# Kernel optimization log

Hardware: AMD Instinct MI355X
Metric: run time of the kernel (lower is better)

The kernel has to match this reference:

```python
import jax, jax.numpy as jnp
import numpy as np

N, D, H, DH = 8192, 512, 8, 64          # seq len, model dim, heads, head dim
NF = int(DH * math_log) if False else 266  # nb_features = int(64 * ln(64)) = 266
EPS = 1e-4                               # performer softmax-kernel eps
LN_EPS = 1e-5


def layernorm(x, g, b):
    mu = x.mean(-1, keepdims=True)
    var = ((x - mu) ** 2).mean(-1, keepdims=True)
    return (x - mu) * jax.lax.rsqrt(var + LN_EPS) * g + b


def softmax_kernel(data, proj, is_query):
    # data: [b,h,n,dh], proj: [nf,dh] -> phi(data): [b,h,n,nf]
    dnorm = DH ** -0.25
    ratio = NF ** -0.5
    dd = jnp.einsum('bhnd,jd->bhnj', data * dnorm, proj)
    diag = (data ** 2).sum(-1, keepdims=True) * 0.5 * (dnorm ** 2)
    if is_query:
        m = jnp.max(dd, axis=-1, keepdims=True)
    else:
        m = jnp.max(dd, axis=(-1, -2), keepdims=True)
    return ratio * (jnp.exp(dd - diag - m) + EPS)


def setup_inputs() -> dict:
    key = jax.random.key(0)
    ks = jax.random.split(key, 10)
    s = 0.02
    return {
        'x': jax.random.normal(ks[0], (N, D), jnp.float32),
        'proj': jax.random.normal(ks[1], (NF, DH), jnp.float32),
        'ln1_g': jnp.ones((D,), jnp.float32), 'ln1_b': jnp.zeros((D,), jnp.float32),
        'wq': jax.random.normal(ks[2], (D, D), jnp.float32) * s,
        'wk': jax.random.normal(ks[3], (D, D), jnp.float32) * s,
        'wv': jax.random.normal(ks[4], (D, D), jnp.float32) * s,
        'wo': jax.random.normal(ks[5], (D, D), jnp.float32) * s,
        'wo_b': jnp.zeros((D,), jnp.float32),
        'ln2_g': jnp.ones((D,), jnp.float32), 'ln2_b': jnp.zeros((D,), jnp.float32),
        'w1': jax.random.normal(ks[6], (D, 4 * D), jnp.float32) * s,
        'b1': jnp.zeros((4 * D,), jnp.float32),
        'w2': jax.random.normal(ks[7], (4 * D, D), jnp.float32) * s,
        'b2': jnp.zeros((D,), jnp.float32),
    }


def reference(x, proj, ln1_g, ln1_b, wq, wk, wv, wo, wo_b, ln2_g, ln2_b, w1, b1, w2, b2):
    xb = x[None]                                     # [1,N,D] (the unsqueeze(0))
    # --- PreLN FAVOR+ self-attention ---
    h = layernorm(xb, ln1_g, ln1_b)
    def split_heads(t):
        return t.reshape(1, N, H, DH).transpose(0, 2, 1, 3)   # [1,H,N,DH]
    q = split_heads(h @ wq)
    k = split_heads(h @ wk)
    v = split_heads(h @ wv)
    qp = softmax_kernel(q, proj, True)               # [1,H,N,NF]
    kp = softmax_kernel(k, proj, False)              # [1,H,N,NF]
    # non-causal linear attention
    context = jnp.einsum('bhnj,bhnd->bhjd', kp, v)   # [1,H,NF,DH]
    d_inv = 1.0 / jnp.einsum('bhnj,bhj->bhn', qp, kp.sum(axis=2))
    attn = jnp.einsum('bhnj,bhjd->bhnd', qp, context) * d_inv[..., None]
    attn = attn.transpose(0, 2, 1, 3).reshape(1, N, D)
    xb = xb + attn @ wo + wo_b
    # --- PreLN feed-forward (GELU, mult=4) ---
    h2 = layernorm(xb, ln2_g, ln2_b)
    xb = xb + jax.nn.gelu(h2 @ w1 + b1) @ w2 + b2
    return xb[0]                                     # squeeze -> [N,D]
```

## Files before the change

### kernel.cpp

```cpp
#include <hip/hip_runtime.h>
#include <math.h>


typedef __attribute__((ext_vector_type(8))) short bf16x8;
typedef __attribute__((ext_vector_type(4))) float f32x4;

#define N_SEQ 8192
#define DMODEL 512
#define DQKV 1536
#define NHEAD 8
#define DHEAD 64
#define NF 266
#define NFP 320
#define PEPS 1e-4f
#define LNEPS 1e-5f
#define RATIO 0.06131393694f

__device__ __forceinline__ unsigned short f2bf(float f) {
  unsigned u = __float_as_uint(f);
  u += 0x7FFFu + ((u >> 16) & 1u);
  return (unsigned short)(u >> 16);
}
__device__ __forceinline__ float bf2f(unsigned short b) {
  return __uint_as_float(((unsigned)b) << 16);
}
__device__ __forceinline__ unsigned enc_f32(float f) {
  unsigned i = __float_as_uint(f);
  return (i & 0x80000000u) ? ~i : (i | 0x80000000u);
}
__device__ __forceinline__ float dec_f32(unsigned u) {
  return (u & 0x80000000u) ? __uint_as_float(u & 0x7FFFFFFFu) : __uint_as_float(~u);
}

__device__ __forceinline__ void g2l16(const void* g, void* l) {
  __builtin_amdgcn_global_load_lds(
      (const __attribute__((address_space(1))) void*)g,
      (__attribute__((address_space(3))) void*)l, 16, 0, 0);
}

template <int N>
__device__ __forceinline__ void wait_vmcnt() {
  if constexpr (N == 0) asm volatile("s_waitcnt vmcnt(0)" ::: "memory");
  else if constexpr (N == 5) asm volatile("s_waitcnt vmcnt(5)" ::: "memory");
  else if constexpr (N == 6) asm volatile("s_waitcnt vmcnt(6)" ::: "memory");
}
__device__ __forceinline__ void wait_lgkm0() {
  asm volatile("s_waitcnt lgkmcnt(0)" ::: "memory");
}


__global__ __launch_bounds__(256) void prep_kernel(
    const float* __restrict__ wq, const float* __restrict__ wk,
    const float* __restrict__ wv, const float* __restrict__ wo,
    const float* __restrict__ w1, const float* __restrict__ w2,
    const float* __restrict__ proj,
    unsigned short* __restrict__ wtqkv, unsigned short* __restrict__ wot,
    unsigned short* __restrict__ w1t, unsigned short* __restrict__ w2t,
    unsigned short* __restrict__ pb, unsigned* __restrict__ mk,
    const float* __restrict__ x,
    const float* __restrict__ ln1g, const float* __restrict__ ln1b,
    unsigned short* __restrict__ h_bf) {
  int bid = blockIdx.x;
  if (bid < 3072) {
    const float* src; unsigned short* dst; int R, C, base;
    if (bid < 256)       { src = wq; dst = wtqkv;          R = 512;  C = 512;  base = 0; }
    else if (bid < 512)  { src = wk; dst = wtqkv + 262144; R = 512;  C = 512;  base = 256; }
    else if (bid < 768)  { src = wv; dst = wtqkv + 524288; R = 512;  C = 512;  base = 512; }
    else if (bid < 1024) { src = wo; dst = wot;            R = 512;  C = 512;  base = 768; }
    else if (bid < 2048) { src = w1; dst = w1t;            R = 512;  C = 2048; base = 1024; }
    else                 { src = w2; dst = w2t;            R = 2048; C = 512;  base = 2048; }
    int lb = bid - base;
    int nbx = C / 32;
    int c0 = (lb % nbx) * 32, r0 = (lb / nbx) * 32;
    __shared__ float tile[32][33];
    int tx = threadIdx.x & 31, ty = threadIdx.x >> 5;
    #pragma unroll
    for (int i = ty; i < 32; i += 8)
      tile[i][tx] = src[(long)(r0 + i) * C + c0 + tx];
    __syncthreads();
    #pragma unroll
    for (int i = ty; i < 32; i += 8)
      dst[(long)(c0 + i) * R + r0 + tx] = f2bf(tile[tx][i]);
  } else if (bid < 3152) {
    int id = (bid - 3072) * 256 + threadIdx.x;
    int j = id >> 6;
    pb[id] = (j < NF) ? f2bf(proj[(long)j * 64 + (id & 63)] * 0.35355339059327373f)
                      : (unsigned short)0;
  } else if (bid == 3152) {
    if (threadIdx.x < NHEAD) mk[threadIdx.x] = 0x007FFFFFu;
  } else {
    __shared__ float sred[4];
    int row = bid - 3153, t = threadIdx.x;
    float2 v = ((const float2*)(x + (long)row * DMODEL))[t];
    float s = v.x + v.y;
    #pragma unroll
    for (int m = 32; m >= 1; m >>= 1) s += __shfl_xor(s, m);
    if ((t & 63) == 0) sred[t >> 6] = s;
    __syncthreads();
    float mu = (sred[0] + sred[1] + sred[2] + sred[3]) * (1.0f / DMODEL);
    __syncthreads();
    float d0 = v.x - mu, d1 = v.y - mu;
    float q = d0 * d0 + d1 * d1;
    #pragma unroll
    for (int m = 32; m >= 1; m >>= 1) q += __shfl_xor(q, m);
    if ((t & 63) == 0) sred[t >> 6] = q;
    __syncthreads();
    float var = (sred[0] + sred[1] + sred[2] + sred[3]) * (1.0f / DMODEL);
    float inv = rsqrtf(var + LNEPS);
    int c = t * 2;
    unsigned short o0 = f2bf(d0 * inv * ln1g[c] + ln1b[c]);
    unsigned short o1 = f2bf(d1 * inv * ln1g[c + 1] + ln1b[c + 1]);
    ((unsigned*)(h_bf + (long)row * DMODEL))[t] = ((unsigned)o1 << 16) | o0;
  }
}


__global__ __launch_bounds__(256) void ln_kernel(const float* __restrict__ x,
                                                 const float* __restrict__ g,
                                                 const float* __restrict__ b,
                                                 unsigned short* __restrict__ out) {
  __shared__ float sred[4];
  int row = blockIdx.x, t = threadIdx.x;
  float2 v = ((const float2*)(x + (long)row * DMODEL))[t];
  float s = v.x + v.y;
  #pragma unroll
  for (int m = 32; m >= 1; m >>= 1) s += __shfl_xor(s, m);
  if ((t & 63) == 0) sred[t >> 6] = s;
  __syncthreads();
  float mu = (sred[0] + sred[1] + sred[2] + sred[3]) * (1.0f / DMODEL);
  __syncthreads();
  float d0 = v.x - mu, d1 = v.y - mu;
  float q = d0 * d0 + d1 * d1;
  #pragma unroll
  for (int m = 32; m >= 1; m >>= 1) q += __shfl_xor(q, m);
  if ((t & 63) == 0) sred[t >> 6] = q;
  __syncthreads();
  float var = (sred[0] + sred[1] + sred[2] + sred[3]) * (1.0f / DMODEL);
  float inv = rsqrtf(var + LNEPS);
  int c = t * 2;
  unsigned short o0 = f2bf(d0 * inv * g[c] + b[c]);
  unsigned short o1 = f2bf(d1 * inv * g[c + 1] + b[c + 1]);
  ((unsigned*)(out + (long)row * DMODEL))[t] = ((unsigned)o1 << 16) | o0;
}

enum { EPI_BF16 = 0, EPI_BIAS_RES_F32 = 2, EPI_BIAS_GELU = 3, EPI_QKV = 4 };


template <int EPI>
__global__ __launch_bounds__(512, 4) void gemm8w_kernel(
    const unsigned short* __restrict__ A, int lda,
    const unsigned short* __restrict__ Bt, int ldb,
    void* __restrict__ Cv, int ldc,
    int K,
    const float* __restrict__ bias,
    const float* __restrict__ res, int ldr,
    unsigned short* __restrict__ vt) {
  constexpr int MR = 4, NR = 2;
  constexpr int S = 5;
  const int tid = threadIdx.x;
  const int wave = tid >> 6, lane = tid & 63;
  const int lr = lane & 15, lg = lane >> 4;
  const int wr = wave >> 1, wc = wave & 1;
  const int m0 = blockIdx.x * 256, n0 = blockIdx.y * 64;

  __shared__ uint4 a_s[2][2048];
  __shared__ uint4 b_s[2][512];

  const unsigned short* asrc[4];
  #pragma unroll
  for (int e = 0; e < 4; ++e) {
    int chunk = e * 512 + tid;
    int r = chunk >> 3, c = chunk & 7;
    asrc[e] = A + (long)(m0 + r) * lda + (c ^ (r & 7)) * 8;
  }
  const unsigned short* bsrc;
  {
    int r = tid >> 3, c = tid & 7;
    bsrc = Bt + (long)(n0 + r) * ldb + (c ^ (r & 7)) * 8;
  }
  const int wbase = tid & 448;

  f32x4 acc[MR][NR] = {};

  auto stage = [&](int buf, int t) {
    #pragma unroll
    for (int e = 0; e < 4; ++e)
      g2l16(asrc[e] + t * 64, &a_s[buf][e * 512 + wbase]);
    g2l16(bsrc + t * 64, &b_s[buf][wbase]);
  };
  auto compute = [&](int buf) {
    #pragma unroll
    for (int ks = 0; ks < 2; ++ks) {
      bf16x8 af[MR], bv[NR];
      #pragma unroll
      for (int i = 0; i < MR; ++i) {
        int r = wr * 64 + i * 16 + lr;
        af[i] = *(const bf16x8*)&a_s[buf][r * 8 + ((ks * 4 + lg) ^ (r & 7))];
      }
      #pragma unroll
      for (int j = 0; j < NR; ++j) {
        int r = wc * 32 + j * 16 + lr;
        bv[j] = *(const bf16x8*)&b_s[buf][r * 8 + ((ks * 4 + lg) ^ (r & 7))];
      }
      #pragma unroll
      for (int i = 0; i < MR; ++i)
        #pragma unroll
        for (int j = 0; j < NR; ++j)
          acc[i][j] = __builtin_amdgcn_mfma_f32_16x16x32_bf16(af[i], bv[j], acc[i][j], 0, 0, 0);
    }
  };

  const int NT = K >> 6;
  stage(0, 0);
  stage(1, 1);
  wait_vmcnt<S>();
  __builtin_amdgcn_s_barrier();

  int cur = 0;
  for (int t = 0; t < NT; ++t) {
    compute(cur);
    if (t + 1 < NT) {
      wait_lgkm0();
      __builtin_amdgcn_s_barrier();
      if (t + 2 < NT) {
        stage(cur, t + 2);
        wait_vmcnt<S>();
      } else {
        wait_vmcnt<0>();
      }
      __builtin_amdgcn_s_barrier();
    }
    cur ^= 1;
  }

  #pragma unroll
  for (int i = 0; i < MR; ++i) {
    #pragma unroll
    for (int j = 0; j < NR; ++j) {
      int gn = n0 + wc * 32 + j * 16 + lr;
      int gm0 = m0 + wr * 64 + i * 16 + lg * 4;
      if (EPI == EPI_QKV && gn >= 1024) {
        int d = gn - 1024;
        uint2 u;
        u.x = (unsigned)f2bf(acc[i][j][0]) | ((unsigned)f2bf(acc[i][j][1]) << 16);
        u.y = (unsigned)f2bf(acc[i][j][2]) | ((unsigned)f2bf(acc[i][j][3]) << 16);
        *(uint2*)(vt + (long)d * N_SEQ + gm0) = u;
        continue;
      }
      #pragma unroll
      for (int rg = 0; rg < 4; ++rg) {
        int gm = gm0 + rg;
        float v = acc[i][j][rg];
        if (EPI == EPI_BF16 || EPI == EPI_QKV) {
          ((unsigned short*)Cv)[(long)gm * ldc + gn] = f2bf(v);
        } else if (EPI == EPI_BIAS_RES_F32) {
          v += bias[gn] + res[(long)gm * ldr + gn];
          ((float*)Cv)[(long)gm * ldc + gn] = v;
        } else if (EPI == EPI_BIAS_GELU) {
          v += bias[gn];
          float t3 = 0.7978845608028654f * (v + 0.044715f * v * v * v);
          v = v / (1.0f + __expf(-2.0f * t3));
          ((unsigned short*)Cv)[(long)gm * ldc + gn] = f2bf(v);
        }
      }
    }
  }
}


template <int BM, int BN, int WM, int WN, int EPI>
__global__ __launch_bounds__(256) void gemm_kernel(
    const unsigned short* __restrict__ A, int lda,
    const unsigned short* __restrict__ Bt, int ldb,
    void* __restrict__ Cv, int ldc,
    int K,
    const float* __restrict__ bias,
    const float* __restrict__ res, int ldr) {
  static_assert((BM / WM) * (BN / WN) == 4, "need 4 waves");
  constexpr int MR = WM / 16, NR = WN / 16;
  constexpr int WNN = BN / WN;
  constexpr int AIT = BM * 8 / 256;
  constexpr int BIT = BN * 8 / 256;
  constexpr int S = AIT + BIT;
  static_assert(S == 6, "wait count tuned for BM=128,BN=64");
  const int tid = threadIdx.x;
  const int wave = tid >> 6, lane = tid & 63;
  const int lr = lane & 15, lg = lane >> 4;
  const int wr = wave / WNN, wc = wave % WNN;
  const int m0 = blockIdx.x * BM, n0 = blockIdx.y * BN;

  __shared__ uint4 a_s[2][BM * 8];
  __shared__ uint4 b_s[2][BN * 8];

  const unsigned short* asrc[AIT];
  #pragma unroll
  for (int e = 0; e < AIT; ++e) {
    int chunk = e * 256 + tid;
    int r = chunk >> 3, c = chunk & 7;
    asrc[e] = A + (long)(m0 + r) * lda + (c ^ (r & 7)) * 8;
  }
  const unsigned short* bsrc[BIT];
  #pragma unroll
  for (int e = 0; e < BIT; ++e) {
    int chunk = e * 256 + tid;
    int r = chunk >> 3, c = chunk & 7;
    bsrc[e] = Bt + (long)(n0 + r) * ldb + (c ^ (r & 7)) * 8;
  }
  const int wbase = tid & 192;

  f32x4 acc[MR][NR] = {};

  auto stage = [&](int buf, int t) {
    #pragma unroll
    for (int e = 0; e < AIT; ++e)
      g2l16(asrc[e] + t * 64, &a_s[buf][e * 256 + wbase]);
    #pragma unroll
    for (int e = 0; e < BIT; ++e)
      g2l16(bsrc[e] + t * 64, &b_s[buf][e * 256 + wbase]);
  };
  auto compute = [&](int buf) {
    #pragma unroll
    for (int ks = 0; ks < 2; ++ks) {
      bf16x8 af[MR], bv[NR];
      #pragma unroll
      for (int i = 0; i < MR; ++i) {
        int r = wr * WM + i * 16 + lr;
        af[i] = *(const bf16x8*)&a_s[buf][r * 8 + ((ks * 4 + lg) ^ (r & 7))];
      }
      #pragma unroll
      for (int j = 0; j < NR; ++j) {
        int r = wc * WN + j * 16 + lr;
        bv[j] = *(const bf16x8*)&b_s[buf][r * 8 + ((ks * 4 + lg) ^ (r & 7))];
      }
      #pragma unroll
      for (int i = 0; i < MR; ++i)
        #pragma unroll
        for (int j = 0; j < NR; ++j)
          acc[i][j] = __builtin_amdgcn_mfma_f32_16x16x32_bf16(af[i], bv[j], acc[i][j], 0, 0, 0);
    }
  };

  const int NT = K >> 6;
  stage(0, 0);
  stage(1, 1);
  wait_vmcnt<6>();
  __builtin_amdgcn_s_barrier();

  int cur = 0;
  for (int t = 0; t < NT; ++t) {
    compute(cur);
    if (t + 1 < NT) {
      wait_lgkm0();
      __builtin_amdgcn_s_barrier();
      if (t + 2 < NT) {
        stage(cur, t + 2);
        wait_vmcnt<6>();
      } else {
        wait_vmcnt<0>();
      }
      __builtin_amdgcn_s_barrier();
    }
    cur ^= 1;
  }

  #pragma unroll
  for (int i = 0; i < MR; ++i) {
    #pragma unroll
    for (int j = 0; j < NR; ++j) {
      int gn = n0 + wc * WN + j * 16 + lr;
      #pragma unroll
      for (int rg = 0; rg < 4; ++rg) {
        int gm = m0 + wr * WM + i * 16 + lg * 4 + rg;
        float v = acc[i][j][rg];
        if (EPI == EPI_BF16) {
          ((unsigned short*)Cv)[(long)gm * ldc + gn] = f2bf(v);
        } else if (EPI == EPI_BIAS_RES_F32) {
          v += bias[gn] + res[(long)gm * ldr + gn];
          ((float*)Cv)[(long)gm * ldc + gn] = v;
        } else if (EPI == EPI_BIAS_GELU) {
          v += bias[gn];
          float t3 = 0.7978845608028654f * (v + 0.044715f * v * v * v);
          v = v / (1.0f + __expf(-2.0f * t3));
          ((unsigned short*)Cv)[(long)gm * ldc + gn] = f2bf(v);
        }
      }
    }
  }
}


__global__ __launch_bounds__(256) void kmax_kernel(
    const unsigned short* __restrict__ Kp,
    const unsigned short* __restrict__ pb,
    unsigned* __restrict__ mk) {
  const int tid = threadIdx.x;
  const int wave = tid >> 6, lane = tid & 63;
  const int lr = lane & 15, lg = lane >> 4;
  const int h = blockIdx.z;
  const int m0 = blockIdx.x * 256;
  const int wbase = tid & 192;

  __shared__ uint4 pbs[2560];
  __shared__ uint4 abuf[2][512];
  __shared__ float sred[4];

  #pragma unroll
  for (int e = 0; e < 10; ++e) {
    int chunk = e * 256 + tid;
    int r = chunk >> 3, c = chunk & 7;
    g2l16(pb + (long)r * DHEAD + (c ^ (r & 7)) * 8, pbs + e * 256 + wbase);
  }
  auto stage_a = [&](int b, int sub) {
    #pragma unroll
    for (int e = 0; e < 2; ++e) {
      int chunk = e * 256 + tid;
      int r = chunk >> 3, c = chunk & 7;
      g2l16(Kp + (long)(m0 + sub * 64 + r) * DQKV + h * DHEAD + (c ^ (r & 7)) * 8,
            abuf[b] + e * 256 + wbase);
    }
  };

  stage_a(0, 0);
  __syncthreads();

  float m = -3.0e38f;
  for (int sub = 0; sub < 4; ++sub) {
    const int cur = sub & 1;
    if (sub + 1 < 4) stage_a(cur ^ 1, sub + 1);

    f32x4 acc[17] = {};
    #pragma unroll
    for (int ks = 0; ks < 2; ++ks) {
      int rA = wave * 16 + lr;
      bf16x8 af = *(const bf16x8*)&abuf[cur][rA * 8 + ((ks * 4 + lg) ^ (rA & 7))];
      #pragma unroll
      for (int j = 0; j < 17; ++j) {
        int rB = j * 16 + lr;
        bf16x8 bv = *(const bf16x8*)&pbs[rB * 8 + ((ks * 4 + lg) ^ (rB & 7))];
        acc[j] = __builtin_amdgcn_mfma_f32_16x16x32_bf16(af, bv, acc[j], 0, 0, 0);
      }
    }
    #pragma unroll
    for (int j = 0; j < 17; ++j) {
      bool valid = (j < 16) || (lr < 10);
      if (valid) {
        #pragma unroll
        for (int rg = 0; rg < 4; ++rg) m = fmaxf(m, acc[j][rg]);
      }
    }
    if (sub + 1 < 4) __syncthreads();
  }

  #pragma unroll
  for (int s = 1; s < 64; s <<= 1) m = fmaxf(m, __shfl_xor(m, s));
  if (lane == 0) sred[wave] = m;
  __syncthreads();
  if (tid == 0) {
    float mm = fmaxf(fmaxf(sred[0], sred[1]), fmaxf(sred[2], sred[3]));
    atomicMax(&mk[h], enc_f32(mm));
  }
}


__global__ __launch_bounds__(256) void ctx_fused_kernel(
    const unsigned short* __restrict__ Kp,
    const unsigned short* __restrict__ pb,
    const unsigned short* __restrict__ vT,
    const unsigned* __restrict__ mk,
    float* __restrict__ part,
    float* __restrict__ kspart) {
  const int tid = threadIdx.x;
  const int wave = tid >> 6, lane = tid & 63;
  const int lr = lane & 15, lg = lane >> 4;
  const int kc = blockIdx.x, h = blockIdx.y;
  const int wbase = tid & 192;

  __shared__ uint4 smem[7168];
  uint4* pbs = smem;
  auto kbuf = [&](int b) { return smem + 2560 + b * 512; };
  auto vbuf = [&](int b) { return smem + 3584 + b * 512; };
  uint4* Pt = smem + 4608;

  #pragma unroll
  for (int e = 0; e < 10; ++e) {
    int chunk = e * 256 + tid;
    int r = chunk >> 3, c = chunk & 7;
    g2l16(pb + (long)r * DHEAD + (c ^ (r & 7)) * 8, pbs + e * 256 + wbase);
  }

  auto stage_kv = [&](int b, int sub) {
    int n0 = kc * 256 + sub * 64;
    #pragma unroll
    for (int e = 0; e < 2; ++e) {
      int chunk = e * 256 + tid;
      int r = chunk >> 3, c = chunk & 7;
      g2l16(Kp + (long)(n0 + r) * DQKV + h * DHEAD + (c ^ (r & 7)) * 8,
            kbuf(b) + e * 256 + wbase);
      g2l16(vT + ((long)h * DHEAD + r) * N_SEQ + n0 + (c ^ (r & 7)) * 8,
            vbuf(b) + e * 256 + wbase);
    }
  };

  const float mh = dec_f32(mk[h]);
  f32x4 acc2[2][10] = {};
  float colacc[20];
  #pragma unroll
  for (int j = 0; j < 20; ++j) colacc[j] = 0.f;

  const int wr = wave >> 1, wc = wave & 1;

  stage_kv(0, 0);
  for (int sub = 0; sub < 4; ++sub) {
    const int cur = sub & 1;
    __syncthreads();
    if (sub + 1 < 4) stage_kv(cur ^ 1, sub + 1);

    f32x4 acc[20] = {};
    float qs = 0.f;
    #pragma unroll
    for (int ks = 0; ks < 2; ++ks) {
      int rA = wave * 16 + lr;
      bf16x8 af = *(const bf16x8*)&kbuf(cur)[rA * 8 + ((ks * 4 + lg) ^ (rA & 7))];
      #pragma unroll
      for (int i = 0; i < 8; ++i) {
        float f = bf2f((unsigned short)af[i]);
        qs += f * f;
      }
      #pragma unroll
      for (int j = 0; j < 20; ++j) {
        int rB = j * 16 + lr;
        bf16x8 bv = *(const bf16x8*)&pbs[rB * 8 + ((ks * 4 + lg) ^ (rB & 7))];
        acc[j] = __builtin_amdgcn_mfma_f32_16x16x32_bf16(af, bv, acc[j], 0, 0, 0);
      }
    }
    qs += __shfl_xor(qs, 16);
    qs += __shfl_xor(qs, 32);
    float dg[4];
    #pragma unroll
    for (int rg = 0; rg < 4; ++rg) dg[rg] = 0.0625f * __shfl(qs, lg * 4 + rg);

    __syncthreads();

    unsigned short* Ptu = (unsigned short*)Pt;
    const int nrow = wave * 16 + lg * 4;
    #pragma unroll
    for (int j = 0; j < 20; ++j) {
      int colj = j * 16 + lr;
      #pragma unroll
      for (int rg = 0; rg < 4; ++rg) {
        float v = 0.f;
        if (colj < NF) v = RATIO * (__expf(acc[j][rg] - dg[rg] - mh) + PEPS);
        colacc[j] += v;
        int nr = nrow + rg;
        int idx = ((colj * 8 + ((nr >> 3) ^ (colj & 7))) << 3) + (nr & 7);
        Ptu[idx] = f2bf(v);
      }
    }
    __syncthreads();

    #pragma unroll
    for (int ks = 0; ks < 2; ++ks) {
      bf16x8 af[2], bv[10];
      #pragma unroll
      for (int i = 0; i < 2; ++i) {
        int r = wr * 32 + i * 16 + lr;
        af[i] = *(const bf16x8*)&vbuf(cur)[r * 8 + ((ks * 4 + lg) ^ (r & 7))];
      }
      #pragma unroll
      for (int j = 0; j < 10; ++j) {
        int r = wc * 160 + j * 16 + lr;
        bv[j] = *(const bf16x8*)&Pt[r * 8 + ((ks * 4 + lg) ^ (r & 7))];
      }
      #pragma unroll
      for (int i = 0; i < 2; ++i)
        #pragma unroll
        for (int j = 0; j < 10; ++j)
          acc2[i][j] = __builtin_amdgcn_mfma_f32_16x16x32_bf16(af[i], bv[j], acc2[i][j], 0, 0, 0);
    }
  }

  float* pbase = part + ((long)(h * 32 + kc)) * 64 * NFP;
  #pragma unroll
  for (int i = 0; i < 2; ++i) {
    #pragma unroll
    for (int j = 0; j < 10; ++j) {
      int gn = wc * 160 + j * 16 + lr;
      #pragma unroll
      for (int rg = 0; rg < 4; ++rg) {
        int gm = wr * 32 + i * 16 + lg * 4 + rg;
        pbase[(long)gm * NFP + gn] = acc2[i][j][rg];
      }
    }
  }

  __syncthreads();
  float* kls = (float*)Pt;
  #pragma unroll
  for (int j = 0; j < 20; ++j) {
    float cs = colacc[j];
    cs += __shfl_xor(cs, 16);
    cs += __shfl_xor(cs, 32);
    if (lg == 0) kls[wave * NFP + j * 16 + lr] = cs;
  }
  __syncthreads();
  for (int c0 = tid; c0 < NFP; c0 += 256) {
    kspart[((long)(h * 32 + kc)) * NFP + c0] =
        kls[c0] + kls[NFP + c0] + kls[2 * NFP + c0] + kls[3 * NFP + c0];
  }
}


__global__ void ctx_reduce_kernel(const float* __restrict__ part,
                                  const float* __restrict__ kspart,
                                  unsigned short* __restrict__ ctxpad) {
  int i = blockIdx.x * 256 + threadIdx.x;
  int h = i / (96 * NFP);
  int rem = i % (96 * NFP);
  int r = rem / NFP, j = rem % NFP;
  float s = 0.f;
  if (r < 64) {
    #pragma unroll 4
    for (int kc = 0; kc < 32; ++kc)
      s += part[((long)(h * 32 + kc)) * 64 * NFP + r * NFP + j];
  } else if (r == 64) {
    #pragma unroll 4
    for (int kc = 0; kc < 32; ++kc)
      s += kspart[((long)(h * 32 + kc)) * NFP + j];
  }
  ctxpad[i] = f2bf(s);
}


__global__ __launch_bounds__(256) void attn_fused_kernel(
    const unsigned short* __restrict__ Qp,
    const unsigned short* __restrict__ pb,
    const unsigned short* __restrict__ ctxpad,
    unsigned short* __restrict__ attn) {
  const int tid = threadIdx.x;
  const int wave = tid >> 6, lane = tid & 63;
  const int lr = lane & 15, lg = lane >> 4;
  const int h = blockIdx.z;
  const int m0 = blockIdx.x * 64;
  const int wbase = tid & 192;

  __shared__ uint4 smem[4096];
  auto sbuf = [&](int b) { return smem + b * 768; };
  uint4* Pf = smem + 1536;

  const unsigned short* Aq = Qp + (long)m0 * DQKV + h * DHEAD;
  const unsigned short* Ch = ctxpad + (long)h * 96 * NFP;

  auto stage_ctx = [&](int b, int kk) {
    #pragma unroll
    for (int e = 0; e < 3; ++e) {
      int chunk = e * 256 + tid;
      int r = chunk >> 3, c = chunk & 7;
      g2l16(Ch + (long)r * NFP + kk * 64 + (c ^ (r & 7)) * 8, sbuf(b) + e * 256 + wbase);
    }
  };

  #pragma unroll
  for (int e = 0; e < 2; ++e) {
    int chunk = e * 256 + tid;
    int r = chunk >> 3, c = chunk & 7;
    g2l16(Aq + (long)r * DQKV + (c ^ (r & 7)) * 8, sbuf(0) + e * 256 + wbase);
  }
  #pragma unroll
  for (int e = 0; e < 10; ++e) {
    int chunk = e * 256 + tid;
    int r = chunk >> 3, c = chunk & 7;
    g2l16(pb + (long)r * DHEAD + (c ^ (r & 7)) * 8, Pf + e * 256 + wbase);
  }
  __syncthreads();

  f32x4 acc[20] = {};
  float qs = 0.f;
  #pragma unroll
  for (int ks = 0; ks < 2; ++ks) {
    int rA = wave * 16 + lr;
    bf16x8 af = *(const bf16x8*)&sbuf(0)[rA * 8 + ((ks * 4 + lg) ^ (rA & 7))];
    #pragma unroll
    for (int i = 0; i < 8; ++i) {
      float f = bf2f((unsigned short)af[i]);
      qs += f * f;
    }
    #pragma unroll
    for (int j = 0; j < 20; ++j) {
      int rB = j * 16 + lr;
      bf16x8 bv = *(const bf16x8*)&Pf[rB * 8 + ((ks * 4 + lg) ^ (rB & 7))];
      acc[j] = __builtin_amdgcn_mfma_f32_16x16x32_bf16(af, bv, acc[j], 0, 0, 0);
    }
  }
  qs += __shfl_xor(qs, 16);
  qs += __shfl_xor(qs, 32);
  float dg[4];
  #pragma unroll
  for (int rg = 0; rg < 4; ++rg) dg[rg] = 0.0625f * __shfl(qs, lg * 4 + rg);

  float mrow[4];
  #pragma unroll
  for (int rg = 0; rg < 4; ++rg) mrow[rg] = -3.0e38f;
  #pragma unroll
  for (int j = 0; j < 17; ++j) {
    bool valid = (j < 16) || (lr < 10);
    if (valid) {
      #pragma unroll
      for (int rg = 0; rg < 4; ++rg) mrow[rg] = fmaxf(mrow[rg], acc[j][rg]);
    }
  }
  #pragma unroll
  for (int s = 1; s < 16; s <<= 1)
    #pragma unroll
    for (int rg = 0; rg < 4; ++rg) mrow[rg] = fmaxf(mrow[rg], __shfl_xor(mrow[rg], s));

  __syncthreads();
  stage_ctx(0, 0);

  unsigned short* Pu = (unsigned short*)Pf;
  const int prow = wave * 16 + lg * 4;
  #pragma unroll
  for (int j = 0; j < 20; ++j) {
    int col = j * 16 + lr;
    int kk = col >> 6, cc = (col >> 3) & 7;
    #pragma unroll
    for (int rg = 0; rg < 4; ++rg) {
      float v = 0.f;
      if (col < NF) v = RATIO * (__expf(acc[j][rg] - dg[rg] - mrow[rg]) + PEPS);
      int rw = prow + rg;
      int idx = ((kk * 512 + rw * 8 + (cc ^ (rw & 7))) << 3) + (col & 7);
      Pu[idx] = f2bf(v);
    }
  }
  __syncthreads();

  f32x4 acc2[6] = {};
  #pragma unroll
  for (int kk = 0; kk < 5; ++kk) {
    const int cur = kk & 1;
    if (kk + 1 < 5) stage_ctx(cur ^ 1, kk + 1);
    #pragma unroll
    for (int ks = 0; ks < 2; ++ks) {
      int rA = wave * 16 + lr;
      bf16x8 af = *(const bf16x8*)&Pf[kk * 512 + rA * 8 + ((ks * 4 + lg) ^ (rA & 7))];
      #pragma unroll
      for (int j = 0; j < 6; ++j) {
        int rB = j * 16 + lr;
        bf16x8 bv = *(const bf16x8*)&sbuf(cur)[rB * 8 + ((ks * 4 + lg) ^ (rB & 7))];
        acc2[j] = __builtin_amdgcn_mfma_f32_16x16x32_bf16(af, bv, acc2[j], 0, 0, 0);
      }
    }
    if (kk + 1 < 5) __syncthreads();
  }

  #pragma unroll
  for (int rg = 0; rg < 4; ++rg) {
    float dv = __shfl(acc2[4][rg], lane & 48);
    float inv = 1.0f / dv;
    int gm = m0 + wave * 16 + lg * 4 + rg;
    #pragma unroll
    for (int j = 0; j < 4; ++j) {
      attn[(long)gm * DMODEL + h * DHEAD + j * 16 + lr] = f2bf(acc2[j][rg] * inv);
    }
  }
}


extern "C" void kernel_launch(void* const* d_in, const int* in_sizes, int n_in,
                              void* d_out, int out_size, void* d_ws, size_t ws_size,
                              hipStream_t stream) {
  const float* x    = (const float*)d_in[0];
  const float* proj = (const float*)d_in[1];
  const float* ln1g = (const float*)d_in[2];
  const float* ln1b = (const float*)d_in[3];
  const float* wq   = (const float*)d_in[4];
  const float* wk   = (const float*)d_in[5];
  const float* wv   = (const float*)d_in[6];
  const float* wo   = (const float*)d_in[7];
  const float* wob  = (const float*)d_in[8];
  const float* ln2g = (const float*)d_in[9];
  const float* ln2b = (const float*)d_in[10];
  const float* w1   = (const float*)d_in[11];
  const float* b1   = (const float*)d_in[12];
  const float* w2   = (const float*)d_in[13];
  const float* b2   = (const float*)d_in[14];

  char* ws = (char*)d_ws;
  unsigned short* wtqkv = (unsigned short*)(ws + 0);
  unsigned short* wot   = (unsigned short*)(ws + 1572864);
  unsigned short* w1t   = (unsigned short*)(ws + 2097152);
  unsigned short* w2t   = (unsigned short*)(ws + 4194304);
  unsigned short* pb    = (unsigned short*)(ws + 6291456);
  unsigned short* h_bf  = (unsigned short*)(ws + 6332416);
  unsigned short* qkv   = (unsigned short*)(ws + 14721024);
  unsigned* mk          = (unsigned*)(ws + 124297216);
  unsigned short* vT    = (unsigned short*)(ws + 124297472);
  float* part           = (float*)(ws + 132686080);
  float* kspart         = (float*)(ws + 153657600);
  unsigned short* ctxpad= (unsigned short*)(ws + 154978560);
  unsigned short* gbf   = (unsigned short*)(ws + 130468096);
  unsigned short* attn  = h_bf;
  unsigned short* h2    = qkv;
  float* xb             = (float*)d_out;

  dim3 blk(256);

  prep_kernel<<<11345, blk, 0, stream>>>(wq, wk, wv, wo, w1, w2, proj,
                                         wtqkv, wot, w1t, w2t, pb, mk,
                                         x, ln1g, ln1b, h_bf);

  gemm8w_kernel<EPI_QKV><<<dim3(32, 24), dim3(512), 0, stream>>>(
      h_bf, 512, wtqkv, 512, qkv, DQKV, 512, nullptr, nullptr, 0, vT);

  kmax_kernel<<<dim3(32, 1, 8), blk, 0, stream>>>(qkv + 512, pb, mk);

  ctx_fused_kernel<<<dim3(32, 8), blk, 0, stream>>>(qkv + 512, pb, vT, mk, part, kspart);
  ctx_reduce_kernel<<<960, blk, 0, stream>>>(part, kspart, ctxpad);

  attn_fused_kernel<<<dim3(128, 1, 8), blk, 0, stream>>>(qkv, pb, ctxpad, attn);

  gemm_kernel<128, 64, 64, 32, EPI_BIAS_RES_F32><<<dim3(64, 8), blk, 0, stream>>>(
      attn, 512, wot, 512, xb, 512, 512, wob, x, 512);

  ln_kernel<<<N_SEQ, blk, 0, stream>>>(xb, ln2g, ln2b, h2);

  gemm8w_kernel<EPI_BIAS_GELU><<<dim3(32, 32), dim3(512), 0, stream>>>(
      h2, 512, w1t, 512, gbf, 2048, 512, b1, nullptr, 0, nullptr);

  gemm8w_kernel<EPI_BIAS_RES_F32><<<dim3(32, 8), dim3(512), 0, stream>>>(
      gbf, 2048, w2t, 2048, d_out, 512, 2048, b2, xb, 512, nullptr);
}
```

Measured before the change: 179.8 us.

## Use wave-per-row layernorm, shrink ctx LDS, switch FFN2 to smaller-tile GEMM

LayerNorm now processes one row per wavefront with float4 loads and shuffle-only reductions, dropping shared-memory syncs and cutting the block count by four. The context kernel drops K/V double buffering and splits the P tile into two halves, shrinking LDS so two blocks can fit per CU, at the cost of losing load/compute overlap. The final FFN down-projection moves from the 8-wave GEMM to the 128x64 tile GEMM, launching more blocks to fill the device better.

After: 168.4 us. 1.07x faster.

```diff
diff --git a/kernel.cpp b/kernel.cpp
--- a/kernel.cpp
+++ b/kernel.cpp
@@ -46,6 +46,38 @@
 }
 __device__ __forceinline__ void wait_lgkm0() {
   asm volatile("s_waitcnt lgkmcnt(0)" ::: "memory");
+}
+
+
+__device__ __forceinline__ void ln_row(const float* __restrict__ x,
+                                       const float* __restrict__ g,
+                                       const float* __restrict__ b,
+                                       unsigned short* __restrict__ out,
+                                       long row, int lane) {
+  const float4* xr = (const float4*)(x + row * DMODEL);
+  float4 v0 = xr[lane * 2], v1 = xr[lane * 2 + 1];
+  float s = v0.x + v0.y + v0.z + v0.w + v1.x + v1.y + v1.z + v1.w;
+  #pragma unroll
+  for (int m = 32; m >= 1; m >>= 1) s += __shfl_xor(s, m);
+  float mu = s * (1.0f / DMODEL);
+  float d[8] = {v0.x - mu, v0.y - mu, v0.z - mu, v0.w - mu,
+                v1.x - mu, v1.y - mu, v1.z - mu, v1.w - mu};
+  float q = 0.f;
+  #pragma unroll
+  for (int k = 0; k < 8; ++k) q += d[k] * d[k];
+  #pragma unroll
+  for (int m = 32; m >= 1; m >>= 1) q += __shfl_xor(q, m);
+  float inv = rsqrtf(q * (1.0f / DMODEL) + LNEPS);
+  const float4* gr = (const float4*)g;
+  const float4* br = (const float4*)b;
+  float4 g0 = gr[lane * 2], g1 = gr[lane * 2 + 1];
+  float4 b0 = br[lane * 2], b1 = br[lane * 2 + 1];
+  float gg[8] = {g0.x, g0.y, g0.z, g0.w, g1.x, g1.y, g1.z, g1.w};
+  float bb[8] = {b0.x, b0.y, b0.z, b0.w, b1.x, b1.y, b1.z, b1.w};
+  unsigned short o[8];
+  #pragma unroll
+  for (int k = 0; k < 8; ++k) o[k] = f2bf(d[k] * inv * gg[k] + bb[k]);
+  ((uint4*)(out + row * DMODEL))[lane] = *(uint4*)o;
 }
 
 
@@ -89,28 +121,8 @@
   } else if (bid == 3152) {
     if (threadIdx.x < NHEAD) mk[threadIdx.x] = 0x007FFFFFu;
   } else {
-    __shared__ float sred[4];
-    int row = bid - 3153, t = threadIdx.x;
-    float2 v = ((const float2*)(x + (long)row * DMODEL))[t];
-    float s = v.x + v.y;
-    #pragma unroll
-    for (int m = 32; m >= 1; m >>= 1) s += __shfl_xor(s, m);
-    if ((t & 63) == 0) sred[t >> 6] = s;
-    __syncthreads();
-    float mu = (sred[0] + sred[1] + sred[2] + sred[3]) * (1.0f / DMODEL);
-    __syncthreads();
-    float d0 = v.x - mu, d1 = v.y - mu;
-    float q = d0 * d0 + d1 * d1;
-    #pragma unroll
-    for (int m = 32; m >= 1; m >>= 1) q += __shfl_xor(q, m);
-    if ((t & 63) == 0) sred[t >> 6] = q;
-    __syncthreads();
-    float var = (sred[0] + sred[1] + sred[2] + sred[3]) * (1.0f / DMODEL);
-    float inv = rsqrtf(var + LNEPS);
-    int c = t * 2;
-    unsigned short o0 = f2bf(d0 * inv * ln1g[c] + ln1b[c]);
-    unsigned short o1 = f2bf(d1 * inv * ln1g[c + 1] + ln1b[c + 1]);
-    ((unsigned*)(h_bf + (long)row * DMODEL))[t] = ((unsigned)o1 << 16) | o0;
+    long row = (long)(bid - 3153) * 4 + (threadIdx.x >> 6);
+    ln_row(x, ln1g, ln1b, h_bf, row, threadIdx.x & 63);
   }
 }
 
@@ -119,28 +131,8 @@
                                                  const float* __restrict__ g,
                                                  const float* __restrict__ b,
                                                  unsigned short* __restrict__ out) {
-  __shared__ float sred[4];
-  int row = blockIdx.x, t = threadIdx.x;
-  float2 v = ((const float2*)(x + (long)row * DMODEL))[t];
-  float s = v.x + v.y;
-  #pragma unroll
-  for (int m = 32; m >= 1; m >>= 1) s += __shfl_xor(s, m);
-  if ((t & 63) == 0) sred[t >> 6] = s;
-  __syncthreads();
-  float mu = (sred[0] + sred[1] + sred[2] + sred[3]) * (1.0f / DMODEL);
-  __syncthreads();
-  float d0 = v.x - mu, d1 = v.y - mu;
-  float q = d0 * d0 + d1 * d1;
-  #pragma unroll
-  for (int m = 32; m >= 1; m >>= 1) q += __shfl_xor(q, m);
-  if ((t & 63) == 0) sred[t >> 6] = q;
-  __syncthreads();
-  float var = (sred[0] + sred[1] + sred[2] + sred[3]) * (1.0f / DMODEL);
-  float inv = rsqrtf(var + LNEPS);
-  int c = t * 2;
-  unsigned short o0 = f2bf(d0 * inv * g[c] + b[c]);
-  unsigned short o1 = f2bf(d1 * inv * g[c + 1] + b[c + 1]);
-  ((unsigned*)(out + (long)row * DMODEL))[t] = ((unsigned)o1 << 16) | o0;
+  long row = (long)blockIdx.x * 4 + (threadIdx.x >> 6);
+  ln_row(x, g, b, out, row, threadIdx.x & 63);
 }
 
 enum { EPI_BF16 = 0, EPI_BIAS_RES_F32 = 2, EPI_BIAS_GELU = 3, EPI_QKV = 4 };
@@ -462,7 +454,7 @@
 }
 
 
-__global__ __launch_bounds__(256) void ctx_fused_kernel(
+__global__ __launch_bounds__(256, 2) void ctx_fused_kernel(
     const unsigned short* __restrict__ Kp,
     const unsigned short* __restrict__ pb,
     const unsigned short* __restrict__ vT,
@@ -475,11 +467,11 @@
   const int kc = blockIdx.x, h = blockIdx.y;
   const int wbase = tid & 192;
 
-  __shared__ uint4 smem[7168];
-  uint4* pbs = smem;
-  auto kbuf = [&](int b) { return smem + 2560 + b * 512; };
-  auto vbuf = [&](int b) { return smem + 3584 + b * 512; };
-  uint4* Pt = smem + 4608;
+  __shared__ uint4 smem[4864];
+  uint4* pbs  = smem;
+  uint4* kstg = smem + 2560;
+  uint4* vstg = smem + 3072;
+  uint4* Pt   = smem + 3584;
 
   #pragma unroll
   for (int e = 0; e < 10; ++e) {
@@ -488,39 +480,34 @@
     g2l16(pb + (long)r * DHEAD + (c ^ (r & 7)) * 8, pbs + e * 256 + wbase);
   }
 
-  auto stage_kv = [&](int b, int sub) {
-    int n0 = kc * 256 + sub * 64;
+  const float mh = dec_f32(mk[h]);
+  f32x4 acc2[2][10] = {};
+  float colacc[20];
+  #pragma unroll
+  for (int j = 0; j < 20; ++j) colacc[j] = 0.f;
+
+  const int wr = wave >> 1, wc = wave & 1;
+
+  for (int sub = 0; sub < 4; ++sub) {
+    const int n0 = kc * 256 + sub * 64;
+    __syncthreads();
     #pragma unroll
     for (int e = 0; e < 2; ++e) {
       int chunk = e * 256 + tid;
       int r = chunk >> 3, c = chunk & 7;
       g2l16(Kp + (long)(n0 + r) * DQKV + h * DHEAD + (c ^ (r & 7)) * 8,
-            kbuf(b) + e * 256 + wbase);
+            kstg + e * 256 + wbase);
       g2l16(vT + ((long)h * DHEAD + r) * N_SEQ + n0 + (c ^ (r & 7)) * 8,
-            vbuf(b) + e * 256 + wbase);
-    }
-  };
-
-  const float mh = dec_f32(mk[h]);
-  f32x4 acc2[2][10] = {};
-  float colacc[20];
-  #pragma unroll
-  for (int j = 0; j < 20; ++j) colacc[j] = 0.f;
-
-  const int wr = wave >> 1, wc = wave & 1;
-
-  stage_kv(0, 0);
-  for (int sub = 0; sub < 4; ++sub) {
-    const int cur = sub & 1;
+            vstg + e * 256 + wbase);
+    }
     __syncthreads();
-    if (sub + 1 < 4) stage_kv(cur ^ 1, sub + 1);
 
     f32x4 acc[20] = {};
     float qs = 0.f;
     #pragma unroll
     for (int ks = 0; ks < 2; ++ks) {
       int rA = wave * 16 + lr;
-      bf16x8 af = *(const bf16x8*)&kbuf(cur)[rA * 8 + ((ks * 4 + lg) ^ (rA & 7))];
+      bf16x8 af = *(const bf16x8*)&kstg[rA * 8 + ((ks * 4 + lg) ^ (rA & 7))];
       #pragma unroll
       for (int i = 0; i < 8; ++i) {
         float f = bf2f((unsigned short)af[i]);
@@ -539,43 +526,47 @@
     #pragma unroll
     for (int rg = 0; rg < 4; ++rg) dg[rg] = 0.0625f * __shfl(qs, lg * 4 + rg);
 
-    __syncthreads();
-
-    unsigned short* Ptu = (unsigned short*)Pt;
-    const int nrow = wave * 16 + lg * 4;
-    #pragma unroll
-    for (int j = 0; j < 20; ++j) {
-      int colj = j * 16 + lr;
-      #pragma unroll
-      for (int rg = 0; rg < 4; ++rg) {
-        float v = 0.f;
-        if (colj < NF) v = RATIO * (__expf(acc[j][rg] - dg[rg] - mh) + PEPS);
-        colacc[j] += v;
-        int nr = nrow + rg;
-        int idx = ((colj * 8 + ((nr >> 3) ^ (colj & 7))) << 3) + (nr & 7);
-        Ptu[idx] = f2bf(v);
-      }
-    }
-    __syncthreads();
-
-    #pragma unroll
-    for (int ks = 0; ks < 2; ++ks) {
-      bf16x8 af[2], bv[10];
-      #pragma unroll
-      for (int i = 0; i < 2; ++i) {
-        int r = wr * 32 + i * 16 + lr;
-        af[i] = *(const bf16x8*)&vbuf(cur)[r * 8 + ((ks * 4 + lg) ^ (r & 7))];
-      }
-      #pragma unroll
-      for (int j = 0; j < 10; ++j) {
-        int r = wc * 160 + j * 16 + lr;
-        bv[j] = *(const bf16x8*)&Pt[r * 8 + ((ks * 4 + lg) ^ (r & 7))];
-      }
-      #pragma unroll
-      for (int i = 0; i < 2; ++i)
+    #pragma unroll
+    for (int hf = 0; hf < 2; ++hf) {
+      __syncthreads();
+      unsigned short* Ptu = (unsigned short*)Pt;
+      const int nrow = wave * 16 + lg * 4;
+      #pragma unroll
+      for (int j = hf * 10; j < hf * 10 + 10; ++j) {
+        int colj = j * 16 + lr;
+        int rloc = colj - hf * 160;
         #pragma unroll
-        for (int j = 0; j < 10; ++j)
-          acc2[i][j] = __builtin_amdgcn_mfma_f32_16x16x32_bf16(af[i], bv[j], acc2[i][j], 0, 0, 0);
+        for (int rg = 0; rg < 4; ++rg) {
+          float v = 0.f;
+          if (colj < NF) v = RATIO * (__expf(acc[j][rg] - dg[rg] - mh) + PEPS);
+          colacc[j] += v;
+          int nr = nrow + rg;
+          int idx = ((rloc * 8 + ((nr >> 3) ^ (rloc & 7))) << 3) + (nr & 7);
+          Ptu[idx] = f2bf(v);
+        }
+      }
+      __syncthreads();
+
+      #pragma unroll
+      for (int ks = 0; ks < 2; ++ks) {
+        bf16x8 af[2], bv[5];
+        #pragma unroll
+        for (int i = 0; i < 2; ++i) {
+          int r = wr * 32 + i * 16 + lr;
+          af[i] = *(const bf16x8*)&vstg[r * 8 + ((ks * 4 + lg) ^ (r & 7))];
+        }
+        #pragma unroll
+        for (int jj = 0; jj < 5; ++jj) {
+          int r = wc * 80 + jj * 16 + lr;
+          bv[jj] = *(const bf16x8*)&Pt[r * 8 + ((ks * 4 + lg) ^ (r & 7))];
+        }
+        #pragma unroll
+        for (int i = 0; i < 2; ++i)
+          #pragma unroll
+          for (int jj = 0; jj < 5; ++jj)
+            acc2[i][hf * 5 + jj] =
+                __builtin_amdgcn_mfma_f32_16x16x32_bf16(af[i], bv[jj], acc2[i][hf * 5 + jj], 0, 0, 0);
+      }
     }
   }
 
@@ -583,12 +574,13 @@
   #pragma unroll
   for (int i = 0; i < 2; ++i) {
     #pragma unroll
-    for (int j = 0; j < 10; ++j) {
-      int gn = wc * 160 + j * 16 + lr;
+    for (int idx = 0; idx < 10; ++idx) {
+      int hf = idx / 5, jj = idx % 5;
+      int gn = hf * 160 + wc * 80 + jj * 16 + lr;
       #pragma unroll
       for (int rg = 0; rg < 4; ++rg) {
         int gm = wr * 32 + i * 16 + lg * 4 + rg;
-        pbase[(long)gm * NFP + gn] = acc2[i][j][rg];
+        pbase[(long)gm * NFP + gn] = acc2[i][idx][rg];
       }
     }
   }
@@ -804,9 +796,9 @@
 
   dim3 blk(256);
 
-  prep_kernel<<<11345, blk, 0, stream>>>(wq, wk, wv, wo, w1, w2, proj,
-                                         wtqkv, wot, w1t, w2t, pb, mk,
-                                         x, ln1g, ln1b, h_bf);
+  prep_kernel<<<5201, blk, 0, stream>>>(wq, wk, wv, wo, w1, w2, proj,
+                                        wtqkv, wot, w1t, w2t, pb, mk,
+                                        x, ln1g, ln1b, h_bf);
 
   gemm8w_kernel<EPI_QKV><<<dim3(32, 24), dim3(512), 0, stream>>>(
       h_bf, 512, wtqkv, 512, qkv, DQKV, 512, nullptr, nullptr, 0, vT);
@@ -821,11 +813,11 @@
   gemm_kernel<128, 64, 64, 32, EPI_BIAS_RES_F32><<<dim3(64, 8), blk, 0, stream>>>(
       attn, 512, wot, 512, xb, 512, 512, wob, x, 512);
 
-  ln_kernel<<<N_SEQ, blk, 0, stream>>>(xb, ln2g, ln2b, h2);
+  ln_kernel<<<2048, blk, 0, stream>>>(xb, ln2g, ln2b, h2);
 
   gemm8w_kernel<EPI_BIAS_GELU><<<dim3(32, 32), dim3(512), 0, stream>>>(
       h2, 512, w1t, 512, gbf, 2048, 512, b1, nullptr, 0, nullptr);
 
-  gemm8w_kernel<EPI_BIAS_RES_F32><<<dim3(32, 8), dim3(512), 0, stream>>>(
-      gbf, 2048, w2t, 2048, d_out, 512, 2048, b2, xb, 512, nullptr);
-}
+  gemm_kernel<128, 64, 64, 32, EPI_BIAS_RES_F32><<<dim3(64, 8), blk, 0, stream>>>(
+      gbf, 2048, w2t, 2048, d_out, 512, 2048, b2, xb, 512);
+}
```
